# Kernel tuning notes

Measured on AMD Instinct MI355X. Metric: run time of the kernel, lower is better.

## Reference

```python
import jax, jax.numpy as jnp
import numpy as np
from jax import lax

N_GAUSS = 4096


def setup_inputs() -> dict:
    key = jax.random.key(0)
    k1, k2, k3, k4 = jax.random.split(key, 4)
    return {
        "_xyz": jax.random.normal(k1, (N_GAUSS, 3), dtype=jnp.float32),
        "_scaling": jax.random.normal(k2, (N_GAUSS, 3), dtype=jnp.float32),
        "_rotation": jax.random.normal(k3, (N_GAUSS, 4), dtype=jnp.float32),
        "_opacity": jax.random.normal(k4, (N_GAUSS, 1), dtype=jnp.float32),
        "resolution": 64,
        "num_blocks": 16,
    }


def _extract_fields(_xyz, _scaling, _rotation, _opacity, resolution, num_blocks):
    relax_ratio = 1.5
    block_size = 2.0 / num_blocks
    split_size = resolution // num_blocks

    # opacity activation + threshold mask (kept dense; masked gaussians get 0 weight)
    opacities = jax.nn.sigmoid(_opacity)[:, 0]  # [N]
    keep = opacities > 0.005
    opa = jnp.where(keep, opacities, 0.0)

    BIG = jnp.float32(1e10)
    mn = jnp.min(jnp.where(keep[:, None], _xyz, BIG), axis=0)
    mx = jnp.max(jnp.where(keep[:, None], _xyz, -BIG), axis=0)
    center = (mn + mx) / 2
    scale = 1.8 / jnp.max(mx - mn)
    xyzs = (_xyz - center) * scale           # [N,3] normalized positions
    stds = jnp.exp(_scaling) * scale         # [N,3] scaling activation * scale

    # covariance from scaling+rotation: L = R @ diag(s); C = L L^T
    q = _rotation / jnp.linalg.norm(_rotation, axis=1, keepdims=True)
    r, x, y, z = q[:, 0], q[:, 1], q[:, 2], q[:, 3]
    R = jnp.stack([
        jnp.stack([1 - 2 * (y * y + z * z), 2 * (x * y - r * z), 2 * (x * z + r * y)], -1),
        jnp.stack([2 * (x * y + r * z), 1 - 2 * (x * x + z * z), 2 * (y * z - r * x)], -1),
        jnp.stack([2 * (x * z - r * y), 2 * (y * z + r * x), 1 - 2 * (x * x + y * y)], -1),
    ], axis=1)                               # [N,3,3]
    L = R * stds[:, None, :]                 # R @ diag(s)
    C = jnp.einsum('nij,nkj->nik', L, L)     # [N,3,3]
    a, b, c = C[:, 0, 0], C[:, 0, 1], C[:, 0, 2]
    d, e, f = C[:, 1, 1], C[:, 1, 2], C[:, 2, 2]

    # analytic 3x3 symmetric inverse (precomputed per gaussian)
    inv_det = 1.0 / (a * d * f + 2 * e * c * b - e * e * a - c * c * d - b * b * f + 1e-24)
    inv_a = (d * f - e * e) * inv_det
    inv_b = (e * c - b * f) * inv_det
    inv_c = (e * b - c * d) * inv_det
    inv_d = (a * f - c * c) * inv_det
    inv_e = (b * c - e * a) * inv_det
    inv_f = (a * d - b * b) * inv_det

    lin = jnp.linspace(-1.0, 1.0, resolution).astype(jnp.float32)
    nb = num_blocks
    bi, bj, bk = jnp.meshgrid(jnp.arange(nb), jnp.arange(nb), jnp.arange(nb), indexing='ij')
    blocks = jnp.stack([bi.ravel(), bj.ravel(), bk.ravel()], axis=1)  # [nb^3, 3]
    off = jnp.arange(split_size)
    relax = block_size * relax_ratio

    def block_val(blk):
        xs = lin[blk[0] * split_size + off]
        ys = lin[blk[1] * split_size + off]
        zs = lin[blk[2] * split_size + off]
        xx, yy, zz = jnp.meshgrid(xs, ys, zs, indexing='ij')
        pts = jnp.stack([xx.ravel(), yy.ravel(), zz.ravel()], axis=-1)  # [S^3, 3]
        vmin = pts.min(0) - relax
        vmax = pts.max(0) + relax
        inside = jnp.all((xyzs < vmax) & (xyzs > vmin), axis=1)  # [N]
        w_opa = jnp.where(inside, opa, 0.0)                      # [N]
        dxyz = pts[:, None, :] - xyzs[None, :, :]                # [S^3, N, 3]
        px, py, pz = dxyz[..., 0], dxyz[..., 1], dxyz[..., 2]
        power = (-0.5 * (px * px * inv_a + py * py * inv_d + pz * pz * inv_f)
                 - px * py * inv_b - px * pz * inv_c - py * pz * inv_e)
        power = jnp.where(power > 0, jnp.float32(-1e10), power)
        val = jnp.sum(w_opa * jnp.exp(power), axis=1)            # [S^3]
        return val.reshape(split_size, split_size, split_size)

    vals = lax.map(block_val, blocks)  # [nb^3, S, S, S]
    occ = (vals.reshape(nb, nb, nb, split_size, split_size, split_size)
               .transpose(0, 3, 1, 4, 2, 5)
               .reshape(resolution, resolution, resolution))
    return occ


def reference(_xyz, _scaling, _rotation, _opacity, resolution, num_blocks):
    return _extract_fields(_xyz, _scaling, _rotation, _opacity, resolution, num_blocks)
```

## Files before the change

kernel.cpp:

```cpp
#include <hip/hip_runtime.h>

#define NG 4096
#define RELAX 0.1875f
#define BINCAP NG
#define CHUNK 512
#define EV_THREADS 512

__device__ __forceinline__ float linf(int i) { return -1.0f + (2.0f/63.0f)*(float)i; }
__device__ __forceinline__ int cperm(int i) { return (i & 1) ? 7 + ((i+1)>>1) : 7 - (i>>1); }

__global__ __launch_bounds__(256) void gm_reduce1(
    const float* __restrict__ xyz, const float* __restrict__ opac,
    float4* __restrict__ pmin, float4* __restrict__ pmax)
{
  __shared__ float s_mn[3][256];
  __shared__ float s_mx[3][256];
  const int tid = threadIdx.x;
  const int g = blockIdx.x*256 + tid;
  float o = opac[g];
  float sig = 1.0f/(1.0f + __expf(-o));
  bool keep = sig > 0.005f;
  float x = xyz[3*g+0], y = xyz[3*g+1], z = xyz[3*g+2];
  s_mn[0][tid] = keep ? x :  1e10f;
  s_mn[1][tid] = keep ? y :  1e10f;
  s_mn[2][tid] = keep ? z :  1e10f;
  s_mx[0][tid] = keep ? x : -1e10f;
  s_mx[1][tid] = keep ? y : -1e10f;
  s_mx[2][tid] = keep ? z : -1e10f;
  __syncthreads();
  for (int s = 128; s > 0; s >>= 1) {
    if (tid < s) {
      #pragma unroll
      for (int k = 0; k < 3; ++k) {
        s_mn[k][tid] = fminf(s_mn[k][tid], s_mn[k][tid+s]);
        s_mx[k][tid] = fmaxf(s_mx[k][tid], s_mx[k][tid+s]);
      }
    }
    __syncthreads();
  }
  if (tid == 0) {
    pmin[blockIdx.x] = make_float4(s_mn[0][0], s_mn[1][0], s_mn[2][0], 0.0f);
    pmax[blockIdx.x] = make_float4(s_mx[0][0], s_mx[1][0], s_mx[2][0], 0.0f);
  }
}

__global__ void gm_reduce2(const float4* __restrict__ pmin,
                           const float4* __restrict__ pmax,
                           float4* __restrict__ cs)
{
  const int lane = threadIdx.x;
  float mn0=1e10f, mn1=1e10f, mn2=1e10f;
  float mx0=-1e10f, mx1=-1e10f, mx2=-1e10f;
  if (lane < 16) {
    float4 a = pmin[lane], b = pmax[lane];
    mn0=a.x; mn1=a.y; mn2=a.z; mx0=b.x; mx1=b.y; mx2=b.z;
  }
  #pragma unroll
  for (int s = 8; s > 0; s >>= 1) {
    mn0 = fminf(mn0, __shfl_down(mn0, s));
    mn1 = fminf(mn1, __shfl_down(mn1, s));
    mn2 = fminf(mn2, __shfl_down(mn2, s));
    mx0 = fmaxf(mx0, __shfl_down(mx0, s));
    mx1 = fmaxf(mx1, __shfl_down(mx1, s));
    mx2 = fmaxf(mx2, __shfl_down(mx2, s));
  }
  if (lane == 0) {
    float rmax = fmaxf(mx0-mn0, fmaxf(mx1-mn1, mx2-mn2));
    *cs = make_float4((mn0+mx0)*0.5f, (mn1+mx1)*0.5f, (mn2+mx2)*0.5f, 1.8f/rmax);
  }
}

__global__ __launch_bounds__(256) void gm_transform(
    const float* __restrict__ xyz, const float* __restrict__ scal,
    const float* __restrict__ rot, const float* __restrict__ opac,
    const float4* __restrict__ cs,
    float4* __restrict__ posopa, float4* __restrict__ invrec)
{
  const int g = blockIdx.x*256 + threadIdx.x;
  const float4 c = *cs;
  float o = opac[g];
  float sig = 1.0f/(1.0f + __expf(-o));
  float opa = (sig > 0.005f) ? sig : 0.0f;
  float xs = (xyz[3*g+0]-c.x)*c.w;
  float ys = (xyz[3*g+1]-c.y)*c.w;
  float zs = (xyz[3*g+2]-c.z)*c.w;
  float sdx = __expf(scal[3*g+0])*c.w;
  float sdy = __expf(scal[3*g+1])*c.w;
  float sdz = __expf(scal[3*g+2])*c.w;
  float qr=rot[4*g+0], qx=rot[4*g+1], qy=rot[4*g+2], qz=rot[4*g+3];
  float qn = 1.0f/sqrtf(qr*qr+qx*qx+qy*qy+qz*qz);
  qr*=qn; qx*=qn; qy*=qn; qz*=qn;
  float R00 = 1.0f-2.0f*(qy*qy+qz*qz), R01 = 2.0f*(qx*qy-qr*qz), R02 = 2.0f*(qx*qz+qr*qy);
  float R10 = 2.0f*(qx*qy+qr*qz), R11 = 1.0f-2.0f*(qx*qx+qz*qz), R12 = 2.0f*(qy*qz-qr*qx);
  float R20 = 2.0f*(qx*qz-qr*qy), R21 = 2.0f*(qy*qz+qr*qx), R22 = 1.0f-2.0f*(qx*qx+qy*qy);
  float L00=R00*sdx, L01=R01*sdy, L02=R02*sdz;
  float L10=R10*sdx, L11=R11*sdy, L12=R12*sdz;
  float L20=R20*sdx, L21=R21*sdy, L22=R22*sdz;
  float a = L00*L00+L01*L01+L02*L02;
  float b = L00*L10+L01*L11+L02*L12;
  float cc= L00*L20+L01*L21+L02*L22;
  float d = L10*L10+L11*L11+L12*L12;
  float e = L10*L20+L11*L21+L12*L22;
  float f = L20*L20+L21*L21+L22*L22;
  float det = a*d*f + 2.0f*e*cc*b - e*e*a - cc*cc*d - b*b*f + 1e-24f;
  float idt = 1.0f/det;
  float ia=(d*f-e*e)*idt, ib=(e*cc-b*f)*idt, ic=(e*b-cc*d)*idt;
  float id=(a*f-cc*cc)*idt, ie=(b*cc-e*a)*idt, iff=(a*d-b*b)*idt;
  posopa[g] = make_float4(xs, ys, zs, opa);
  invrec[2*g+0] = make_float4(-0.5f*ia, -ib, -ic, -0.5f*id);
  invrec[2*g+1] = make_float4(-ie, -0.5f*iff, 0.0f, 0.0f);
}

__global__ __launch_bounds__(256) void gm_bin(
    const float4* __restrict__ posopa,
    int* __restrict__ bincnt, unsigned short* __restrict__ binidx)
{
  __shared__ int s_cnt;
  __shared__ unsigned short s_idx[NG];
  const int tid = threadIdx.x;
  const int b = blockIdx.x;
  const int bi = b >> 4, bj = b & 15;
  const float vminx = linf(bi*4) - RELAX, vmaxx = linf(bi*4+3) + RELAX;
  const float vminy = linf(bj*4) - RELAX, vmaxy = linf(bj*4+3) + RELAX;
  if (tid == 0) s_cnt = 0;
  __syncthreads();
  #pragma unroll
  for (int t = 0; t < NG/256; ++t) {
    int g = t*256 + tid;
    float4 P = posopa[g];
    if (P.w > 0.0f &&
        P.x > vminx && P.x < vmaxx &&
        P.y > vminy && P.y < vmaxy) {
      int slot = atomicAdd(&s_cnt, 1);
      s_idx[slot] = (unsigned short)g;
    }
  }
  __syncthreads();
  const int n = s_cnt;
  if (tid == 0) bincnt[b] = n;
  for (int t = tid; t < n; t += 256) binidx[b*BINCAP + t] = s_idx[t];
}

__global__ __launch_bounds__(EV_THREADS) void gm_evaluate(
    const float4* __restrict__ posopa, const float4* __restrict__ invrec,
    const int* __restrict__ bincnt, const unsigned short* __restrict__ binidx,
    float* __restrict__ out)
{
  __shared__ int    s_cnt;
  __shared__ float4 s_g[CHUNK*3];
  __shared__ float  s_acc[EV_THREADS];
  const int tid = threadIdx.x;
  const int b = blockIdx.x;
  const int bi = cperm(b >> 8), bj = cperm((b >> 4) & 15), bk = cperm(b & 15);
  const float vminz = linf(bk*4) - RELAX, vmaxz = linf(bk*4+3) + RELAX;
  const int p    = tid & 63;
  const int part = tid >> 6;
  const int sx = p >> 4, sy = (p >> 2) & 3, sz = p & 3;
  const float ptx = linf(bi*4+sx), pty = linf(bj*4+sy), ptz = linf(bk*4+sz);
  const unsigned short* mylist = binidx + (bi*16 + bj)*BINCAP;
  const int nxy = bincnt[bi*16 + bj];
  float acc = 0.0f;

  for (int c0 = 0; c0 < nxy; c0 += CHUNK) {
    if (tid == 0) s_cnt = 0;
    __syncthreads();
    const int lim = min(nxy - c0, CHUNK);
    if (tid < lim) {
      int g = mylist[c0 + tid];
      float4 P = posopa[g];
      if (P.z > vminz && P.z < vmaxz) {
        int slot = atomicAdd(&s_cnt, 1);
        s_g[3*slot+0] = P;
        s_g[3*slot+1] = invrec[2*g+0];
        s_g[3*slot+2] = invrec[2*g+1];
      }
    }
    __syncthreads();
    const int n = s_cnt;
    #pragma unroll 4
    for (int j = part; j < n; j += 8) {
      float4 P  = s_g[3*j+0];
      float4 I0 = s_g[3*j+1];
      float4 I1 = s_g[3*j+2];
      float px = ptx - P.x, py = pty - P.y, pz = ptz - P.z;
      float power = px*px*I0.x + py*py*I0.w + pz*pz*I1.y
                  + px*py*I0.y + px*pz*I0.z + py*pz*I1.x;
      power = (power > 0.0f) ? -1e10f : power;
      acc += P.w * __expf(power);
    }
    __syncthreads();
  }

  s_acc[tid] = acc;
  __syncthreads();
  if (tid < 64) {
    float v = 0.0f;
    #pragma unroll
    for (int w = 0; w < 8; ++w) v += s_acc[tid + w*64];
    out[(bi*4+sx)*4096 + (bj*4+sy)*64 + (bk*4+sz)] = v;
  }
}

__global__ __launch_bounds__(EV_THREADS) void gm_evaluate_nobin(
    const float4* __restrict__ posopa, const float4* __restrict__ invrec,
    float* __restrict__ out)
{
  __shared__ int    s_cnt;
  __shared__ float4 s_g[CHUNK*3];
  __shared__ float  s_acc[EV_THREADS];
  const int tid = threadIdx.x;
  const int b = blockIdx.x;
  const int bi = cperm(b >> 8), bj = cperm((b >> 4) & 15), bk = cperm(b & 15);
  const float vminx = linf(bi*4) - RELAX, vmaxx = linf(bi*4+3) + RELAX;
  const float vminy = linf(bj*4) - RELAX, vmaxy = linf(bj*4+3) + RELAX;
  const float vminz = linf(bk*4) - RELAX, vmaxz = linf(bk*4+3) + RELAX;
  const int p    = tid & 63;
  const int part = tid >> 6;
  const int sx = p >> 4, sy = (p >> 2) & 3, sz = p & 3;
  const float ptx = linf(bi*4+sx), pty = linf(bj*4+sy), ptz = linf(bk*4+sz);
  float acc = 0.0f;
  for (int c0 = 0; c0 < NG; c0 += CHUNK) {
    if (tid == 0) s_cnt = 0;
    __syncthreads();
    int g = c0 + tid;
    float4 P = posopa[g];
    if (P.w > 0.0f &&
        P.x > vminx && P.x < vmaxx &&
        P.y > vminy && P.y < vmaxy &&
        P.z > vminz && P.z < vmaxz) {
      int slot = atomicAdd(&s_cnt, 1);
      s_g[3*slot+0] = P;
      s_g[3*slot+1] = invrec[2*g+0];
      s_g[3*slot+2] = invrec[2*g+1];
    }
    __syncthreads();
    const int n = s_cnt;
    #pragma unroll 4
    for (int j = part; j < n; j += 8) {
      float4 Pq = s_g[3*j+0];
      float4 I0 = s_g[3*j+1];
      float4 I1 = s_g[3*j+2];
      float px = ptx - Pq.x, py = pty - Pq.y, pz = ptz - Pq.z;
      float power = px*px*I0.x + py*py*I0.w + pz*pz*I1.y
                  + px*py*I0.y + px*pz*I0.z + py*pz*I1.x;
      power = (power > 0.0f) ? -1e10f : power;
      acc += Pq.w * __expf(power);
    }
    __syncthreads();
  }
  s_acc[tid] = acc;
  __syncthreads();
  if (tid < 64) {
    float v = 0.0f;
    #pragma unroll
    for (int w = 0; w < 8; ++w) v += s_acc[tid + w*64];
    out[(bi*4+sx)*4096 + (bj*4+sy)*64 + (bk*4+sz)] = v;
  }
}

extern "C" void kernel_launch(void* const* d_in, const int* in_sizes, int n_in,
                              void* d_out, int out_size, void* d_ws, size_t ws_size,
                              hipStream_t stream) {
  const float* xyz  = (const float*)d_in[0];
  const float* scal = (const float*)d_in[1];
  const float* rot  = (const float*)d_in[2];
  const float* opac = (const float*)d_in[3];
  float* out = (float*)d_out;
  char* ws = (char*)d_ws;
  float4* posopa = (float4*)(ws);
  float4* invrec = (float4*)(ws + 65536);
  float4* cs     = (float4*)(ws + 65536 + 131072);
  float4* pmin   = cs + 1;
  float4* pmax   = pmin + 16;
  int*    bincnt = (int*)(pmax + 16);
  unsigned short* binidx = (unsigned short*)(bincnt + 256);
  const size_t needed = 65536 + 131072 + 16 + 512 + 1024 + (size_t)256*BINCAP*2;

  gm_reduce1  <<<16, 256, 0, stream>>>(xyz, opac, pmin, pmax);
  gm_reduce2  <<<1,   64, 0, stream>>>(pmin, pmax, cs);
  gm_transform<<<16, 256, 0, stream>>>(xyz, scal, rot, opac, cs, posopa, invrec);
  if (ws_size >= needed) {
    gm_bin     <<<256, 256, 0, stream>>>(posopa, bincnt, binidx);
    gm_evaluate<<<4096, EV_THREADS, 0, stream>>>(posopa, invrec, bincnt, binidx, out);
  } else {
    gm_evaluate_nobin<<<4096, EV_THREADS, 0, stream>>>(posopa, invrec, out);
  }
}
```

Before: 119.4 us.

## Fuse preprocessing kernels and bin gaussians into full 3D blocks

Merges the two reduction kernels and the transform into one kernel in which each of 8 blocks redundantly recomputes the global min/max before transforming its own slice, removing two launches. Binning now goes to per-(x,y,z) block lists, so the evaluate kernel no longer refilters the xy list by z with shared atomics. Each chunk then loads only relevant gaussians with one fewer barrier. Bin lists are capped at 4096 or 2048 entries depending on workspace size, which could drop gaussians if the smaller cap overflows, and the workspace needed grows to about 32 MB.

```diff
diff --git a/kernel.cpp b/kernel.cpp
--- a/kernel.cpp
+++ b/kernel.cpp
@@ -2,33 +2,38 @@
 
 #define NG 4096
 #define RELAX 0.1875f
-#define BINCAP NG
 #define CHUNK 512
 #define EV_THREADS 512
 
 __device__ __forceinline__ float linf(int i) { return -1.0f + (2.0f/63.0f)*(float)i; }
 __device__ __forceinline__ int cperm(int i) { return (i & 1) ? 7 + ((i+1)>>1) : 7 - (i>>1); }
 
-__global__ __launch_bounds__(256) void gm_reduce1(
-    const float* __restrict__ xyz, const float* __restrict__ opac,
-    float4* __restrict__ pmin, float4* __restrict__ pmax)
-{
-  __shared__ float s_mn[3][256];
-  __shared__ float s_mx[3][256];
-  const int tid = threadIdx.x;
-  const int g = blockIdx.x*256 + tid;
-  float o = opac[g];
-  float sig = 1.0f/(1.0f + __expf(-o));
-  bool keep = sig > 0.005f;
-  float x = xyz[3*g+0], y = xyz[3*g+1], z = xyz[3*g+2];
-  s_mn[0][tid] = keep ? x :  1e10f;
-  s_mn[1][tid] = keep ? y :  1e10f;
-  s_mn[2][tid] = keep ? z :  1e10f;
-  s_mx[0][tid] = keep ? x : -1e10f;
-  s_mx[1][tid] = keep ? y : -1e10f;
-  s_mx[2][tid] = keep ? z : -1e10f;
-  __syncthreads();
-  for (int s = 128; s > 0; s >>= 1) {
+__global__ __launch_bounds__(512) void gm_prep(
+    const float* __restrict__ xyz, const float* __restrict__ scal,
+    const float* __restrict__ rot, const float* __restrict__ opac,
+    float4* __restrict__ posopa, float4* __restrict__ invrec)
+{
+  __shared__ float s_mn[3][512];
+  __shared__ float s_mx[3][512];
+  const int tid = threadIdx.x;
+  float mn0=1e10f, mn1=1e10f, mn2=1e10f;
+  float mx0=-1e10f, mx1=-1e10f, mx2=-1e10f;
+  #pragma unroll
+  for (int t = 0; t < NG/512; ++t) {
+    int g = t*512 + tid;
+    float o = opac[g];
+    float sig = 1.0f/(1.0f + __expf(-o));
+    bool keep = sig > 0.005f;
+    float x = xyz[3*g+0], y = xyz[3*g+1], z = xyz[3*g+2];
+    if (keep) {
+      mn0 = fminf(mn0, x); mn1 = fminf(mn1, y); mn2 = fminf(mn2, z);
+      mx0 = fmaxf(mx0, x); mx1 = fmaxf(mx1, y); mx2 = fmaxf(mx2, z);
+    }
+  }
+  s_mn[0][tid]=mn0; s_mn[1][tid]=mn1; s_mn[2][tid]=mn2;
+  s_mx[0][tid]=mx0; s_mx[1][tid]=mx1; s_mx[2][tid]=mx2;
+  __syncthreads();
+  for (int s = 256; s > 0; s >>= 1) {
     if (tid < s) {
       #pragma unroll
       for (int k = 0; k < 3; ++k) {
@@ -38,55 +43,23 @@
     }
     __syncthreads();
   }
-  if (tid == 0) {
-    pmin[blockIdx.x] = make_float4(s_mn[0][0], s_mn[1][0], s_mn[2][0], 0.0f);
-    pmax[blockIdx.x] = make_float4(s_mx[0][0], s_mx[1][0], s_mx[2][0], 0.0f);
-  }
-}
-
-__global__ void gm_reduce2(const float4* __restrict__ pmin,
-                           const float4* __restrict__ pmax,
-                           float4* __restrict__ cs)
-{
-  const int lane = threadIdx.x;
-  float mn0=1e10f, mn1=1e10f, mn2=1e10f;
-  float mx0=-1e10f, mx1=-1e10f, mx2=-1e10f;
-  if (lane < 16) {
-    float4 a = pmin[lane], b = pmax[lane];
-    mn0=a.x; mn1=a.y; mn2=a.z; mx0=b.x; mx1=b.y; mx2=b.z;
-  }
-  #pragma unroll
-  for (int s = 8; s > 0; s >>= 1) {
-    mn0 = fminf(mn0, __shfl_down(mn0, s));
-    mn1 = fminf(mn1, __shfl_down(mn1, s));
-    mn2 = fminf(mn2, __shfl_down(mn2, s));
-    mx0 = fmaxf(mx0, __shfl_down(mx0, s));
-    mx1 = fmaxf(mx1, __shfl_down(mx1, s));
-    mx2 = fmaxf(mx2, __shfl_down(mx2, s));
-  }
-  if (lane == 0) {
-    float rmax = fmaxf(mx0-mn0, fmaxf(mx1-mn1, mx2-mn2));
-    *cs = make_float4((mn0+mx0)*0.5f, (mn1+mx1)*0.5f, (mn2+mx2)*0.5f, 1.8f/rmax);
-  }
-}
-
-__global__ __launch_bounds__(256) void gm_transform(
-    const float* __restrict__ xyz, const float* __restrict__ scal,
-    const float* __restrict__ rot, const float* __restrict__ opac,
-    const float4* __restrict__ cs,
-    float4* __restrict__ posopa, float4* __restrict__ invrec)
-{
-  const int g = blockIdx.x*256 + threadIdx.x;
-  const float4 c = *cs;
+  const float cx = (s_mn[0][0]+s_mx[0][0])*0.5f;
+  const float cy = (s_mn[1][0]+s_mx[1][0])*0.5f;
+  const float cz = (s_mn[2][0]+s_mx[2][0])*0.5f;
+  const float rmax = fmaxf(s_mx[0][0]-s_mn[0][0],
+                     fmaxf(s_mx[1][0]-s_mn[1][0], s_mx[2][0]-s_mn[2][0]));
+  const float sc = 1.8f/rmax;
+
+  const int g = blockIdx.x*512 + tid;
   float o = opac[g];
   float sig = 1.0f/(1.0f + __expf(-o));
   float opa = (sig > 0.005f) ? sig : 0.0f;
-  float xs = (xyz[3*g+0]-c.x)*c.w;
-  float ys = (xyz[3*g+1]-c.y)*c.w;
-  float zs = (xyz[3*g+2]-c.z)*c.w;
-  float sdx = __expf(scal[3*g+0])*c.w;
-  float sdy = __expf(scal[3*g+1])*c.w;
-  float sdz = __expf(scal[3*g+2])*c.w;
+  float xs = (xyz[3*g+0]-cx)*sc;
+  float ys = (xyz[3*g+1]-cy)*sc;
+  float zs = (xyz[3*g+2]-cz)*sc;
+  float sdx = __expf(scal[3*g+0])*sc;
+  float sdy = __expf(scal[3*g+1])*sc;
+  float sdz = __expf(scal[3*g+2])*sc;
   float qr=rot[4*g+0], qx=rot[4*g+1], qy=rot[4*g+2], qz=rot[4*g+3];
   float qn = 1.0f/sqrtf(qr*qr+qx*qx+qy*qy+qz*qz);
   qr*=qn; qx*=qn; qy*=qn; qz*=qn;
@@ -111,18 +84,17 @@
   invrec[2*g+1] = make_float4(-ie, -0.5f*iff, 0.0f, 0.0f);
 }
 
-__global__ __launch_bounds__(256) void gm_bin(
+__global__ __launch_bounds__(256) void gm_bin3(
     const float4* __restrict__ posopa,
-    int* __restrict__ bincnt, unsigned short* __restrict__ binidx)
-{
-  __shared__ int s_cnt;
-  __shared__ unsigned short s_idx[NG];
+    int* __restrict__ bincnt, unsigned short* __restrict__ binidx, int cap)
+{
+  __shared__ int s_cnt[16];
   const int tid = threadIdx.x;
   const int b = blockIdx.x;
   const int bi = b >> 4, bj = b & 15;
   const float vminx = linf(bi*4) - RELAX, vmaxx = linf(bi*4+3) + RELAX;
   const float vminy = linf(bj*4) - RELAX, vmaxy = linf(bj*4+3) + RELAX;
-  if (tid == 0) s_cnt = 0;
+  if (tid < 16) s_cnt[tid] = 0;
   __syncthreads();
   #pragma unroll
   for (int t = 0; t < NG/256; ++t) {
@@ -131,54 +103,51 @@
     if (P.w > 0.0f &&
         P.x > vminx && P.x < vmaxx &&
         P.y > vminy && P.y < vmaxy) {
-      int slot = atomicAdd(&s_cnt, 1);
-      s_idx[slot] = (unsigned short)g;
-    }
-  }
-  __syncthreads();
-  const int n = s_cnt;
-  if (tid == 0) bincnt[b] = n;
-  for (int t = tid; t < n; t += 256) binidx[b*BINCAP + t] = s_idx[t];
+      #pragma unroll
+      for (int bk = 0; bk < 16; ++bk) {
+        const float lo = linf(bk*4) - RELAX, hi = linf(bk*4+3) + RELAX;
+        if (P.z > lo && P.z < hi) {
+          int slot = atomicAdd(&s_cnt[bk], 1);
+          if (slot < cap)
+            binidx[(size_t)((b<<4) + bk)*cap + slot] = (unsigned short)g;
+        }
+      }
+    }
+  }
+  __syncthreads();
+  if (tid < 16) bincnt[(b<<4) + tid] = min(s_cnt[tid], cap);
 }
 
 __global__ __launch_bounds__(EV_THREADS) void gm_evaluate(
     const float4* __restrict__ posopa, const float4* __restrict__ invrec,
     const int* __restrict__ bincnt, const unsigned short* __restrict__ binidx,
-    float* __restrict__ out)
-{
-  __shared__ int    s_cnt;
+    int cap, float* __restrict__ out)
+{
   __shared__ float4 s_g[CHUNK*3];
   __shared__ float  s_acc[EV_THREADS];
   const int tid = threadIdx.x;
   const int b = blockIdx.x;
   const int bi = cperm(b >> 8), bj = cperm((b >> 4) & 15), bk = cperm(b & 15);
-  const float vminz = linf(bk*4) - RELAX, vmaxz = linf(bk*4+3) + RELAX;
+  const int bin = (bi*16 + bj)*16 + bk;
   const int p    = tid & 63;
   const int part = tid >> 6;
   const int sx = p >> 4, sy = (p >> 2) & 3, sz = p & 3;
   const float ptx = linf(bi*4+sx), pty = linf(bj*4+sy), ptz = linf(bk*4+sz);
-  const unsigned short* mylist = binidx + (bi*16 + bj)*BINCAP;
-  const int nxy = bincnt[bi*16 + bj];
+  const unsigned short* mylist = binidx + (size_t)bin*cap;
+  const int n = bincnt[bin];
   float acc = 0.0f;
 
-  for (int c0 = 0; c0 < nxy; c0 += CHUNK) {
-    if (tid == 0) s_cnt = 0;
-    __syncthreads();
-    const int lim = min(nxy - c0, CHUNK);
+  for (int c0 = 0; c0 < n; c0 += CHUNK) {
+    const int lim = min(n - c0, CHUNK);
     if (tid < lim) {
       int g = mylist[c0 + tid];
-      float4 P = posopa[g];
-      if (P.z > vminz && P.z < vmaxz) {
-        int slot = atomicAdd(&s_cnt, 1);
-        s_g[3*slot+0] = P;
-        s_g[3*slot+1] = invrec[2*g+0];
-        s_g[3*slot+2] = invrec[2*g+1];
-      }
-    }
-    __syncthreads();
-    const int n = s_cnt;
+      s_g[3*tid+0] = posopa[g];
+      s_g[3*tid+1] = invrec[2*g+0];
+      s_g[3*tid+2] = invrec[2*g+1];
+    }
+    __syncthreads();
     #pragma unroll 4
-    for (int j = part; j < n; j += 8) {
+    for (int j = part; j < lim; j += 8) {
       float4 P  = s_g[3*j+0];
       float4 I0 = s_g[3*j+1];
       float4 I1 = s_g[3*j+2];
@@ -269,19 +238,19 @@
   char* ws = (char*)d_ws;
   float4* posopa = (float4*)(ws);
   float4* invrec = (float4*)(ws + 65536);
-  float4* cs     = (float4*)(ws + 65536 + 131072);
-  float4* pmin   = cs + 1;
-  float4* pmax   = pmin + 16;
-  int*    bincnt = (int*)(pmax + 16);
-  unsigned short* binidx = (unsigned short*)(bincnt + 256);
-  const size_t needed = 65536 + 131072 + 16 + 512 + 1024 + (size_t)256*BINCAP*2;
-
-  gm_reduce1  <<<16, 256, 0, stream>>>(xyz, opac, pmin, pmax);
-  gm_reduce2  <<<1,   64, 0, stream>>>(pmin, pmax, cs);
-  gm_transform<<<16, 256, 0, stream>>>(xyz, scal, rot, opac, cs, posopa, invrec);
-  if (ws_size >= needed) {
-    gm_bin     <<<256, 256, 0, stream>>>(posopa, bincnt, binidx);
-    gm_evaluate<<<4096, EV_THREADS, 0, stream>>>(posopa, invrec, bincnt, binidx, out);
+  int*    bincnt = (int*)(ws + 65536 + 131072);
+  unsigned short* binidx = (unsigned short*)(ws + 65536 + 131072 + 16384);
+  const size_t base = 65536 + 131072 + 16384;
+
+  gm_prep<<<8, 512, 0, stream>>>(xyz, scal, rot, opac, posopa, invrec);
+
+  int cap = 0;
+  if      (ws_size >= base + (size_t)4096*4096*2) cap = 4096;
+  else if (ws_size >= base + (size_t)4096*2048*2) cap = 2048;
+
+  if (cap) {
+    gm_bin3    <<<256, 256, 0, stream>>>(posopa, bincnt, binidx, cap);
+    gm_evaluate<<<4096, EV_THREADS, 0, stream>>>(posopa, invrec, bincnt, binidx, cap, out);
   } else {
     gm_evaluate_nobin<<<4096, EV_THREADS, 0, stream>>>(posopa, invrec, out);
   }
```

Result: slower. 142.4 us (+19.3%).
